# Optimization experiments

Hardware: AMD Instinct MI355X
Metric: run time of the kernel (lower is better)

## Reference

```python
import jax, jax.numpy as jnp
import numpy as np

B, T, D, H = 2, 2048, 2048, 16
HD = D // H  # head dim = 128


def setup_inputs() -> dict:
    key = jax.random.key(0)
    k_x, k_qkv, k_out, k_doc = jax.random.split(key, 4)
    x = jax.random.normal(k_x, (B, T, D), dtype=jnp.float32)
    # real RoPE tables (sin/cos of position * inv_freq), shape (T, HD)
    inv_freq = 1.0 / (10000.0 ** (jnp.arange(0, HD, 2, dtype=jnp.float32) / HD))
    ang = jnp.arange(T, dtype=jnp.float32)[:, None] * inv_freq[None, :]  # (T, HD/2)
    ang = jnp.concatenate([ang, ang], axis=-1)  # (T, HD)
    sin, cos = jnp.sin(ang), jnp.cos(ang)
    W_qkv = jax.random.normal(k_qkv, (D, 3 * D), dtype=jnp.float32) * 0.02
    W_out = jax.random.normal(k_out, (D, D), dtype=jnp.float32) * 0.02
    # sorted doc ids per row -> contiguous packed documents
    doc_ids = jnp.sort(jax.random.randint(k_doc, (B, T), 0, 8), axis=-1).astype(jnp.int32)
    return {"x": x, "sin": sin, "cos": cos, "W_qkv": W_qkv, "W_out": W_out, "doc_ids": doc_ids}


def _apply_rope(xh, sin, cos):
    # xh: (B, T, H, HD); sin/cos: (T, HD) broadcast over batch & heads
    s = sin[None, :, None, :]
    c = cos[None, :, None, :]
    x1, x2 = jnp.split(xh, 2, axis=-1)
    rot = jnp.concatenate([-x2, x1], axis=-1)  # rotate_half
    return xh * c + rot * s


def reference(x, sin, cos, W_qkv, W_out, doc_ids):
    b, t, d = x.shape
    qkv = x @ W_qkv  # (B, T, 3D), fused QKV projection, no bias
    q, k, v = jnp.split(qkv, 3, axis=-1)
    q = q.reshape(b, t, H, HD)
    k = k.reshape(b, t, H, HD)
    v = v.reshape(b, t, H, HD)
    q = _apply_rope(q, sin, cos)
    k = _apply_rope(k, sin, cos)
    # doc-causal additive bias: (B, 1, T, T)
    neg_inf = jnp.finfo(q.dtype).min / 2
    causal = jnp.tril(jnp.ones((t, t), dtype=jnp.bool_))
    same_doc = doc_ids[:, :, None] == doc_ids[:, None, :]
    mask = (causal[None, :, :] & same_doc)[:, None, :, :]
    bias = jnp.where(mask, 0.0, neg_inf).astype(q.dtype)
    # attention (matches jax.nn.dot_product_attention with additive bias)
    scale = 1.0 / jnp.sqrt(jnp.asarray(HD, dtype=q.dtype))
    scores = jnp.einsum("bqhd,bkhd->bhqk", q, k) * scale + bias
    attn = jax.nn.softmax(scores, axis=-1)
    out = jnp.einsum("bhqk,bkhd->bqhd", attn, v)  # (B, T, H, HD)
    out = out.reshape(b, t, d)
    return out @ W_out
```

## Files before the change

kernel.cpp:

```cpp
#include <hip/hip_runtime.h>
#include <hip/hip_bf16.h>

#define BB 2
#define TT 2048
#define DD 2048
#define HH 16
#define HDIM 128
#define BT 4096
#define N3 6144

typedef __attribute__((ext_vector_type(8))) short s16x8;
typedef __attribute__((ext_vector_type(4))) float f32x4;

static __device__ __forceinline__ ushort f2bf(float x) {
  union { float f; unsigned u; } cv; cv.f = x;
  unsigned r = cv.u + 0x7FFF + ((cv.u >> 16) & 1);
  return (ushort)(r >> 16);
}
static __device__ __forceinline__ float bf2f(ushort u) {
  union { unsigned u; float f; } cv; cv.u = ((unsigned)u) << 16; return cv.f;
}

#define GLDS16(gp, lp) __builtin_amdgcn_global_load_lds( \
    (const __attribute__((address_space(1))) void*)(gp), \
    (__attribute__((address_space(3))) void*)(lp), 16, 0, 0)

__global__ void cvt_kernel(const float* __restrict__ in, ushort* __restrict__ out, int n4) {
  int i = blockIdx.x * blockDim.x + threadIdx.x;
  if (i < n4) {
    float4 v = ((const float4*)in)[i];
    ushort4 o;
    o.x = f2bf(v.x); o.y = f2bf(v.y); o.z = f2bf(v.z); o.w = f2bf(v.w);
    ((ushort4*)out)[i] = o;
  }
}

__global__ void transpose_cvt(const float* __restrict__ in, ushort* __restrict__ out, int R, int C) {
  __shared__ float tile[32][33];
  const int bx = blockIdx.x * 32, by = blockIdx.y * 32;
  const int tx = threadIdx.x, ty = threadIdx.y;
  #pragma unroll
  for (int i = 0; i < 32; i += 8)
    tile[ty + i][tx] = in[(size_t)(by + ty + i) * C + bx + tx];
  __syncthreads();
  #pragma unroll
  for (int i = 0; i < 32; i += 8)
    out[(size_t)(bx + ty + i) * R + by + tx] = f2bf(tile[tx][ty + i]);
}

template<int MODE>
__global__ __launch_bounds__(256, 2)
void gemm_bt(const ushort* __restrict__ A, const ushort* __restrict__ Bt,
             ushort* __restrict__ Qb, ushort* __restrict__ Kb, ushort* __restrict__ Vb,
             float* __restrict__ Cf, int M, int N, int K)
{
  __shared__ ushort As[128 * 32];
  __shared__ ushort Bs[128 * 32];
  const int tid = threadIdx.x;
  const int wave = tid >> 6, lane = tid & 63;
  const int lr = lane & 15, lg = lane >> 4;
  const int m0 = blockIdx.y * 128, n0 = blockIdx.x * 128;
  const int wm = (wave & 1) * 64, wn = (wave >> 1) * 64;
  f32x4 acc[4][4] = {};

  for (int k0 = 0; k0 < K; k0 += 32) {
    __syncthreads();
    #pragma unroll
    for (int call = 0; call < 2; ++call) {
      const int base = call * 256 + wave * 64;
      const int c = base + lane;
      const int row = c >> 2, cc = c & 3;
      GLDS16(A  + (size_t)(m0 + row) * K + k0 + cc * 8, As + (size_t)base * 8);
      GLDS16(Bt + (size_t)(n0 + row) * K + k0 + cc * 8, Bs + (size_t)base * 8);
    }
    __syncthreads();
    s16x8 a[4], b[4];
    #pragma unroll
    for (int i = 0; i < 4; ++i) a[i] = *(const s16x8*)&As[(wm + i * 16 + lr) * 32 + lg * 8];
    #pragma unroll
    for (int i = 0; i < 4; ++i) b[i] = *(const s16x8*)&Bs[(wn + i * 16 + lr) * 32 + lg * 8];
    #pragma unroll
    for (int mi = 0; mi < 4; ++mi)
      #pragma unroll
      for (int ni = 0; ni < 4; ++ni)
        acc[mi][ni] = __builtin_amdgcn_mfma_f32_16x16x32_bf16(a[mi], b[ni], acc[mi][ni], 0, 0, 0);
  }

  #pragma unroll
  for (int mi = 0; mi < 4; ++mi) {
    #pragma unroll
    for (int ni = 0; ni < 4; ++ni) {
      #pragma unroll
      for (int r = 0; r < 4; ++r) {
        const int row = m0 + wm + mi * 16 + lg * 4 + r;
        const int col = n0 + wn + ni * 16 + lr;
        const float v = acc[mi][ni][r];
        if (MODE == 1) {
          const int which = col >> 11, rem = col & 2047;
          const int hh = rem >> 7, d = rem & 127;
          const int bb = row >> 11, t = row & 2047;
          ushort* dst = (which == 0) ? Qb : (which == 1) ? Kb : Vb;
          dst[(((size_t)bb * HH + hh) * TT + t) * HDIM + d] = f2bf(v);
        } else {
          Cf[(size_t)row * N + col] = v;
        }
      }
    }
  }
}

__global__ void rope_inplace(ushort* __restrict__ Qb, ushort* __restrict__ Kb,
                             const float* __restrict__ sinp, const float* __restrict__ cosp) {
  const int idx = blockIdx.x * 256 + threadIdx.x;
  const int d = idx & 63;
  const int t = (idx >> 6) & (TT - 1);
  const int bh = idx >> 17;
  const float c = cosp[t * HDIM + d];
  const float s = sinp[t * HDIM + d];
  const size_t base = ((size_t)bh * TT + t) * HDIM + d;
  float q1 = bf2f(Qb[base]), q2 = bf2f(Qb[base + 64]);
  Qb[base]      = f2bf(q1 * c - q2 * s);
  Qb[base + 64] = f2bf(q2 * c + q1 * s);
  float k1 = bf2f(Kb[base]), k2 = bf2f(Kb[base + 64]);
  Kb[base]      = f2bf(k1 * c - k2 * s);
  Kb[base + 64] = f2bf(k2 * c + k1 * s);
}

__global__ __launch_bounds__(256, 2)
void attn_kernel(const ushort* __restrict__ Qb, const ushort* __restrict__ Kb,
                 const ushort* __restrict__ Vb, const int* __restrict__ doc,
                 ushort* __restrict__ Ob)
{
  __shared__ ushort Ks[64 * 128];
  __shared__ ushort VTs[128 * 64];
  __shared__ ushort Ps[4][16 * 64];
  const int qt = blockIdx.x, h = blockIdx.y, b = blockIdx.z;
  const int q0 = qt * 64;
  const int tid = threadIdx.x, wave = tid >> 6, lane = tid & 63;
  const int lr = lane & 15, lg = lane >> 4;
  const size_t bh = (size_t)b * HH + h;
  const int* docb = doc + b * TT;

  const ushort* Qp = Qb + (bh * TT + q0 + wave * 16) * HDIM;
  s16x8 aq[4];
  #pragma unroll
  for (int ks = 0; ks < 4; ++ks) aq[ks] = *(const s16x8*)&Qp[lr * HDIM + ks * 32 + lg * 8];

  int qdoc[4];
  #pragma unroll
  for (int r = 0; r < 4; ++r) qdoc[r] = docb[q0 + wave * 16 + lg * 4 + r];
  const int qdoc0 = docb[q0];

  float m2[4], lsum[4];
  #pragma unroll
  for (int r = 0; r < 4; ++r) { m2[r] = -1e30f; lsum[r] = 0.f; }
  f32x4 oacc[8] = {};

  const float sc = 0.08838834764831843f * 1.4426950408889634f;

  const ushort* Kbase = Kb + bh * TT * HDIM;
  const ushort* Vbase = Vb + bh * TT * HDIM;

  const int ntiles = qt + 1;
  for (int kt = 0; kt < ntiles; ++kt) {
    const int kv0 = kt * 64;
    if (docb[kv0 + 63] < qdoc0) continue;
    __syncthreads();
    #pragma unroll
    for (int i = 0; i < 4; ++i) {
      const int c = tid + i * 256;
      const int row = c >> 4, c8 = c & 15;
      s16x8 v = *(const s16x8*)&Kbase[(size_t)(kv0 + row) * HDIM + c8 * 8];
      const int off = (row * 256 + c8 * 16) ^ ((row & 7) << 4);
      *(s16x8*)((char*)Ks + off) = v;
    }
    #pragma unroll
    for (int i = 0; i < 4; ++i) {
      const int c = tid + i * 256;
      const int kv = c >> 4, d8 = c & 15;
      s16x8 v = *(const s16x8*)&Vbase[(size_t)(kv0 + kv) * HDIM + d8 * 8];
      #pragma unroll
      for (int j = 0; j < 8; ++j) {
        const int d = d8 * 8 + j;
        const int off = (d * 128 + kv * 2) ^ ((d & 7) << 4);
        *(ushort*)((char*)VTs + off) = (ushort)v[j];
      }
    }
    __syncthreads();

    f32x4 sfrag[4] = {};
    #pragma unroll
    for (int ks = 0; ks < 4; ++ks) {
      #pragma unroll
      for (int ct = 0; ct < 4; ++ct) {
        const int row = ct * 16 + lr;
        const int off = (row * 256 + ks * 64 + lg * 16) ^ ((row & 7) << 4);
        s16x8 bk = *(const s16x8*)((char*)Ks + off);
        sfrag[ct] = __builtin_amdgcn_mfma_f32_16x16x32_bf16(aq[ks], bk, sfrag[ct], 0, 0, 0);
      }
    }

    int kd[4];
    #pragma unroll
    for (int ct = 0; ct < 4; ++ct) kd[ct] = docb[kv0 + ct * 16 + lr];

    float s[4][4], tmax[4];
    #pragma unroll
    for (int r = 0; r < 4; ++r) tmax[r] = -1e30f;
    #pragma unroll
    for (int ct = 0; ct < 4; ++ct) {
      const int col = kv0 + ct * 16 + lr;
      #pragma unroll
      for (int r = 0; r < 4; ++r) {
        const int row = q0 + wave * 16 + lg * 4 + r;
        float v = sfrag[ct][r] * sc;
        const bool keep = (col <= row) && (kd[ct] == qdoc[r]);
        v = keep ? v : -1e30f;
        s[ct][r] = v;
        tmax[r] = fmaxf(tmax[r], v);
      }
    }
    #pragma unroll
    for (int r = 0; r < 4; ++r) {
      #pragma unroll
      for (int off = 8; off >= 1; off >>= 1)
        tmax[r] = fmaxf(tmax[r], __shfl_xor(tmax[r], off, 16));
    }
    float alpha[4];
    #pragma unroll
    for (int r = 0; r < 4; ++r) {
      const float mnew = fmaxf(m2[r], tmax[r]);
      alpha[r] = exp2f(m2[r] - mnew);
      m2[r] = mnew;
      lsum[r] *= alpha[r];
    }
    #pragma unroll
    for (int ct = 0; ct < 4; ++ct) {
      #pragma unroll
      for (int r = 0; r < 4; ++r) {
        const float p = (s[ct][r] > -1e29f) ? exp2f(s[ct][r] - m2[r]) : 0.f;
        lsum[r] += p;
        const int prow = lg * 4 + r;
        const int off = (prow * 128 + (ct * 16 + lr) * 2) ^ ((prow & 7) << 4);
        *(ushort*)((char*)&Ps[wave][0] + off) = f2bf(p);
      }
    }
    #pragma unroll
    for (int oc = 0; oc < 8; ++oc)
      #pragma unroll
      for (int r = 0; r < 4; ++r) oacc[oc][r] *= alpha[r];
    #pragma unroll
    for (int ks = 0; ks < 2; ++ks) {
      const int poff = (lr * 128 + ks * 64 + lg * 16) ^ ((lr & 7) << 4);
      s16x8 ap = *(const s16x8*)((char*)&Ps[wave][0] + poff);
      #pragma unroll
      for (int oc = 0; oc < 8; ++oc) {
        const int vrow = oc * 16 + lr;
        const int voff = (vrow * 128 + ks * 64 + lg * 16) ^ ((vrow & 7) << 4);
        s16x8 bv = *(const s16x8*)((char*)VTs + voff);
        oacc[oc] = __builtin_amdgcn_mfma_f32_16x16x32_bf16(ap, bv, oacc[oc], 0, 0, 0);
      }
    }
  }

  #pragma unroll
  for (int r = 0; r < 4; ++r)
    #pragma unroll
    for (int off = 8; off >= 1; off >>= 1)
      lsum[r] += __shfl_xor(lsum[r], off, 16);

  ushort* Op = Ob + ((size_t)b * TT + q0 + wave * 16) * DD + (size_t)h * HDIM;
  #pragma unroll
  for (int oc = 0; oc < 8; ++oc)
    #pragma unroll
    for (int r = 0; r < 4; ++r)
      Op[(lg * 4 + r) * DD + oc * 16 + lr] = f2bf(oacc[oc][r] / lsum[r]);
}

extern "C" void kernel_launch(void* const* d_in, const int* in_sizes, int n_in,
                              void* d_out, int out_size, void* d_ws, size_t ws_size,
                              hipStream_t stream)
{
  const float* x    = (const float*)d_in[0];
  const float* sinp = (const float*)d_in[1];
  const float* cosp = (const float*)d_in[2];
  const float* Wqkv = (const float*)d_in[3];
  const float* Wout = (const float*)d_in[4];
  const int*   doc  = (const int*)d_in[5];
  float* out = (float*)d_out;

  ushort* xb  = (ushort*)d_ws;
  ushort* WqT = xb  + (size_t)BT * DD;
  ushort* WoT = WqT + (size_t)N3 * DD;
  ushort* Qb  = WoT + (size_t)DD * DD;
  ushort* Kb  = Qb  + (size_t)BB * TT * DD;
  ushort* Vb  = Kb  + (size_t)BB * TT * DD;
  ushort* Ob  = Vb  + (size_t)BB * TT * DD;

  cvt_kernel<<<(BT * DD / 4 + 255) / 256, 256, 0, stream>>>(x, xb, BT * DD / 4);
  transpose_cvt<<<dim3(N3 / 32, DD / 32), dim3(32, 8), 0, stream>>>(Wqkv, WqT, DD, N3);
  transpose_cvt<<<dim3(DD / 32, DD / 32), dim3(32, 8), 0, stream>>>(Wout, WoT, DD, DD);
  gemm_bt<1><<<dim3(N3 / 128, BT / 128), 256, 0, stream>>>(xb, WqT, Qb, Kb, Vb, nullptr, BT, N3, DD);
  rope_inplace<<<BB * HH * TT * 64 / 256, 256, 0, stream>>>(Qb, Kb, sinp, cosp);
  attn_kernel<<<dim3(TT / 64, HH, BB), 256, 0, stream>>>(Qb, Kb, Vb, doc, Ob);
  gemm_bt<2><<<dim3(DD / 128, BT / 128), 256, 0, stream>>>(Ob, WoT, nullptr, nullptr, nullptr, out, BT, DD, DD);
}
```

Before: 405.1 us.

## Add 256x256 multi-stage pipelined QKV GEMM with swizzled LDS and XCD-aware tiling

Replaces the simple 128x128 single-buffered QKV projection GEMM with a 512-thread, 256x256-tile kernel. It uses a double-buffered 128KB LDS pipeline with asynchronous global-to-LDS loads issued several stages ahead, an XOR swizzle to avoid LDS bank conflicts, and a workgroup remap that spreads tiles across XCDs. The goal is to hide global memory latency and raise MFMA utilisation in the largest GEMM. The cost is occupancy of one workgroup per CU, heavy register use, and only 384 workgroups, which may underfill the CUs. The output GEMM is split into its own fp32-only kernel.

```diff
diff --git a/kernel.cpp b/kernel.cpp
--- a/kernel.cpp
+++ b/kernel.cpp
@@ -48,11 +48,109 @@
     out[(size_t)(bx + ty + i) * R + by + tx] = f2bf(tile[tx][ty + i]);
 }
 
-template<int MODE>
+__global__ __launch_bounds__(512, 1)
+void gemm8_qkv(const ushort* __restrict__ A, const ushort* __restrict__ Bt,
+               ushort* __restrict__ Qb, ushort* __restrict__ Kb, ushort* __restrict__ Vb)
+{
+  constexpr int K = 2048;
+  constexpr int NT = K / 64;
+  constexpr int NBX = N3 / 256;
+  constexpr int NWG = NBX * (BT / 256);
+  __shared__ char smem[131072];
+
+  const int tid = threadIdx.x, wave = tid >> 6, lane = tid & 63;
+  const int lr = lane & 15, lg = lane >> 4;
+  const int wm = wave >> 2, wn = wave & 3;
+
+  const int wg = blockIdx.x;
+  const int nw = (wg & 7) * (NWG / 8) + (wg >> 3);
+  const int by = nw / NBX, bx = nw - by * NBX;
+  const int m0 = by * 256, n0 = bx * 256;
+
+  auto STAGE = [&](int s) {
+    if (s >= 4 * NT) return;
+    const int U = s >> 2, j = s & 3;
+    const int ab = j & 1, ks = j >> 1;
+    const ushort* src = ab ? Bt : A;
+    const int base0 = ab ? n0 : m0;
+    char* dst = smem + (((U & 1) << 16) | (ab << 15) | (ks << 14));
+    #pragma unroll
+    for (int inst = 0; inst < 2; ++inst) {
+      const int c = inst * 512 + tid;
+      const int row = c >> 2;
+      const int colb = (c & 3) * 16;
+      const int colsw = colb ^ (((row >> 2) & 3) << 4);
+      const ushort* gp = src + (size_t)(base0 + row) * K + U * 64 + ks * 32 + (colsw >> 1);
+      GLDS16(gp, dst + inst * 8192 + wave * 1024);
+    }
+  };
+
+  f32x4 acc[8][4] = {};
+
+  #pragma unroll
+  for (int s = 0; s < 6; ++s) STAGE(s);
+  asm volatile("s_waitcnt vmcnt(8)" ::: "memory");
+  __builtin_amdgcn_s_barrier();
+
+  for (int T = 0; T < NT; ++T) {
+    const int buf = T & 1;
+    s16x8 a[8];
+    #pragma unroll
+    for (int p = 0; p < 4; ++p) {
+      const int ks = p >> 1, qn = p & 1;
+      const char* Ab = smem + ((buf << 16) | (ks << 14));
+      const char* Bb = smem + ((buf << 16) | 32768 | (ks << 14));
+      if ((p & 1) == 0) {
+        #pragma unroll
+        for (int mf = 0; mf < 8; ++mf) {
+          const int row = wm * 128 + mf * 16 + lr;
+          a[mf] = *(const s16x8*)(Ab + row * 64 + ((lg * 16) ^ (((row >> 2) & 3) << 4)));
+        }
+      }
+      s16x8 bb[2];
+      #pragma unroll
+      for (int nf = 0; nf < 2; ++nf) {
+        const int row = wn * 64 + qn * 32 + nf * 16 + lr;
+        bb[nf] = *(const s16x8*)(Bb + row * 64 + ((lg * 16) ^ (((row >> 2) & 3) << 4)));
+      }
+      STAGE(4 * T + p + 6);
+      if (p & 1) asm volatile("s_waitcnt vmcnt(8)" ::: "memory");
+      __builtin_amdgcn_s_barrier();
+      asm volatile("s_waitcnt lgkmcnt(0)" ::: "memory");
+      __builtin_amdgcn_sched_barrier(0);
+      __builtin_amdgcn_s_setprio(1);
+      #pragma unroll
+      for (int mf = 0; mf < 8; ++mf)
+        #pragma unroll
+        for (int nf = 0; nf < 2; ++nf)
+          acc[mf][qn * 2 + nf] =
+            __builtin_amdgcn_mfma_f32_16x16x32_bf16(a[mf], bb[nf], acc[mf][qn * 2 + nf], 0, 0, 0);
+      __builtin_amdgcn_s_setprio(0);
+      __builtin_amdgcn_s_barrier();
+    }
+  }
+
+  #pragma unroll
+  for (int mf = 0; mf < 8; ++mf) {
+    #pragma unroll
+    for (int nn = 0; nn < 4; ++nn) {
+      #pragma unroll
+      for (int r = 0; r < 4; ++r) {
+        const int rowg = m0 + wm * 128 + mf * 16 + lg * 4 + r;
+        const int colg = n0 + wn * 64 + nn * 16 + lr;
+        const int which = colg >> 11, rem = colg & 2047;
+        const int hh = rem >> 7, d = rem & 127;
+        const int b2 = rowg >> 11, t = rowg & 2047;
+        ushort* dstp = (which == 0) ? Qb : (which == 1) ? Kb : Vb;
+        dstp[(((size_t)b2 * HH + hh) * TT + t) * HDIM + d] = f2bf(acc[mf][nn][r]);
+      }
+    }
+  }
+}
+
 __global__ __launch_bounds__(256, 2)
-void gemm_bt(const ushort* __restrict__ A, const ushort* __restrict__ Bt,
-             ushort* __restrict__ Qb, ushort* __restrict__ Kb, ushort* __restrict__ Vb,
-             float* __restrict__ Cf, int M, int N, int K)
+void gemm_bt2(const ushort* __restrict__ A, const ushort* __restrict__ Bt,
+              float* __restrict__ Cf, int M, int N, int K)
 {
   __shared__ ushort As[128 * 32];
   __shared__ ushort Bs[128 * 32];
@@ -87,26 +185,15 @@
   }
 
   #pragma unroll
-  for (int mi = 0; mi < 4; ++mi) {
-    #pragma unroll
-    for (int ni = 0; ni < 4; ++ni) {
+  for (int mi = 0; mi < 4; ++mi)
+    #pragma unroll
+    for (int ni = 0; ni < 4; ++ni)
       #pragma unroll
       for (int r = 0; r < 4; ++r) {
         const int row = m0 + wm + mi * 16 + lg * 4 + r;
         const int col = n0 + wn + ni * 16 + lr;
-        const float v = acc[mi][ni][r];
-        if (MODE == 1) {
-          const int which = col >> 11, rem = col & 2047;
-          const int hh = rem >> 7, d = rem & 127;
-          const int bb = row >> 11, t = row & 2047;
-          ushort* dst = (which == 0) ? Qb : (which == 1) ? Kb : Vb;
-          dst[(((size_t)bb * HH + hh) * TT + t) * HDIM + d] = f2bf(v);
-        } else {
-          Cf[(size_t)row * N + col] = v;
-        }
-      }
-    }
-  }
+        Cf[(size_t)row * N + col] = acc[mi][ni][r];
+      }
 }
 
 __global__ void rope_inplace(ushort* __restrict__ Qb, ushort* __restrict__ Kb,
@@ -300,8 +387,8 @@
   cvt_kernel<<<(BT * DD / 4 + 255) / 256, 256, 0, stream>>>(x, xb, BT * DD / 4);
   transpose_cvt<<<dim3(N3 / 32, DD / 32), dim3(32, 8), 0, stream>>>(Wqkv, WqT, DD, N3);
   transpose_cvt<<<dim3(DD / 32, DD / 32), dim3(32, 8), 0, stream>>>(Wout, WoT, DD, DD);
-  gemm_bt<1><<<dim3(N3 / 128, BT / 128), 256, 0, stream>>>(xb, WqT, Qb, Kb, Vb, nullptr, BT, N3, DD);
+  gemm8_qkv<<<dim3((N3 / 256) * (BT / 256)), 512, 0, stream>>>(xb, WqT, Qb, Kb, Vb);
   rope_inplace<<<BB * HH * TT * 64 / 256, 256, 0, stream>>>(Qb, Kb, sinp, cosp);
   attn_kernel<<<dim3(TT / 64, HH, BB), 256, 0, stream>>>(Qb, Kb, Vb, doc, Ob);
-  gemm_bt<2><<<dim3(DD / 128, BT / 128), 256, 0, stream>>>(Ob, WoT, nullptr, nullptr, nullptr, out, BT, DD, DD);
-}
+  gemm_bt2<<<dim3(DD / 128, BT / 128), 256, 0, stream>>>(Ob, WoT, out, BT, DD, DD);
+}
```

Result: no change. 406.3 us (+0.3%).
